# Kernel optimization log

Measured on AMD Instinct MI355X. Metric: run time of the kernel, lower is better.

Reference implementation:

```python
import jax, jax.numpy as jnp
import numpy as np

NUM_HEADS = 14
SCALE = 0.125  # fixed constant in the source, not 1/sqrt(head_dim)
PATCH = 14
DIM = 3 * PATCH * PATCH  # 588


def setup_inputs() -> dict:
    key = jax.random.key(0)
    k_x, k_cw, k_cb, k_qw, k_qb = jax.random.split(key, 5)
    B, C_in, H, W = 8, 3, 448, 448
    x = jax.random.normal(k_x, (B, C_in, H, W), dtype=jnp.float32)
    # Conv2d(in_channels=3, dim, kernel=patch, stride=patch), torch layout OIHW
    fan_in = C_in * PATCH * PATCH
    bound = 1.0 / np.sqrt(fan_in)
    conv_w = jax.random.uniform(k_cw, (DIM, C_in, PATCH, PATCH), jnp.float32, -bound, bound)
    conv_b = jax.random.uniform(k_cb, (DIM,), jnp.float32, -bound, bound)
    # Linear(dim, 3*dim): weight [out, in] torch layout
    lb = 1.0 / np.sqrt(DIM)
    qkv_w = jax.random.uniform(k_qw, (3 * DIM, DIM), jnp.float32, -lb, lb)
    qkv_b = jax.random.uniform(k_qb, (3 * DIM,), jnp.float32, -lb, lb)
    return {"x": x, "conv_w": conv_w, "conv_b": conv_b, "qkv_w": qkv_w, "qkv_b": qkv_b}


def reference(x, conv_w, conv_b, qkv_w, qkv_b):
    # Patch embedding: conv kernel==stride==patch  -> [B, DIM, H/p, W/p]
    y = jax.lax.conv_general_dilated(
        x, conv_w, window_strides=(PATCH, PATCH), padding="VALID",
        dimension_numbers=("NCHW", "OIHW", "NCHW"))
    y = y + conv_b[None, :, None, None]
    B = y.shape[0]
    # flatten(2).transpose(1, 2) -> [B, N, C]
    tokens = y.reshape(B, DIM, -1).transpose(0, 2, 1)
    N, C = tokens.shape[1], tokens.shape[2]
    hd = C // NUM_HEADS  # 42
    qkv = tokens @ qkv_w.T + qkv_b  # [B, N, 3C]
    qkv = qkv.reshape(B, N, 3, NUM_HEADS, hd).transpose(2, 0, 3, 1, 4)  # [3,B,H,N,hd]
    q, k, v = qkv[0], qkv[1], qkv[2]
    attn = jnp.einsum("bhnd,bhmd->bhnm", q, k) * SCALE  # [B,H,N,N]
    attn = jax.nn.softmax(attn, axis=-1)
    out = jnp.einsum("bhnm,bhmd->bhnd", attn, v)  # [B,H,N,hd]
    out = out.transpose(0, 2, 1, 3).reshape(B, N, C)  # [B,N,C]
    return out
```

## Files before the change

kernel.cpp:

```cpp
#include <hip/hip_runtime.h>

typedef unsigned short u16;
typedef unsigned int u32;
typedef __attribute__((ext_vector_type(8))) short bf16x8;
typedef __attribute__((ext_vector_type(4))) float f32x4;

#define MTOK 8192
#define KP   640
#define CC   588
#define C3   1764
#define NH   14
#define SEQ  1024
#define HD   42
#define DP   64
#define DV   48
#define SC2f 0.18033688011112042f

static __device__ __forceinline__ u16 f2b(float f) {
  unsigned u = __builtin_bit_cast(unsigned, f);
  u = (u + 0x7FFFu + ((u >> 16) & 1u)) >> 16;
  return (u16)u;
}

static __device__ __forceinline__ void gl_lds16(const void* g, void* l) {
  auto gp = (const unsigned int __attribute__((address_space(1)))*)((unsigned long long)g);
  auto lp = (unsigned int __attribute__((address_space(3)))*)((unsigned long long)l);
  __builtin_amdgcn_global_load_lds(gp, lp, 16, 0, 0);
}

static __device__ __forceinline__ u32 pk2(float lo, float hi) {
  u32 a = __builtin_bit_cast(u32, lo) + 0x8000u;
  u32 b = __builtin_bit_cast(u32, hi) + 0x8000u;
  return __builtin_amdgcn_perm(b, a, 0x07060302u);
}

__global__ void im2col_k(const float* __restrict__ x, u16* __restrict__ A) {
  int t = blockIdx.x;
  int b = t >> 10, pi = t & 1023, ph = pi >> 5, pw = pi & 31;
  const float* xb = x + (size_t)b * 3 * 448 * 448;
  for (int kk = threadIdx.x; kk < KP; kk += 256) {
    float v = 0.f;
    if (kk < CC) {
      int c = kk / 196, rem = kk - c * 196, i = rem / 14, j = rem - i * 14;
      v = xb[(size_t)(c * 448 + ph * 14 + i) * 448 + pw * 14 + j];
    }
    A[(size_t)t * KP + kk] = f2b(v);
  }
}

__global__ void padw_k(const float* __restrict__ w, u16* __restrict__ dst, int R) {
  int r = blockIdx.x;
  for (int c = threadIdx.x; c < KP; c += 256) {
    float v = (r < R && c < CC) ? w[(size_t)r * CC + c] : 0.f;
    dst[(size_t)r * KP + c] = f2b(v);
  }
}

template <int MODE>
__global__ void __launch_bounds__(256, 2) gemm_k(
    const u16* __restrict__ A, const u16* __restrict__ Bt,
    const float* __restrict__ bias, u16* __restrict__ out0,
    u16* __restrict__ qb, u16* __restrict__ kb, u16* __restrict__ vb) {
  __shared__ alignas(16) u16 sA[128 * 64];
  __shared__ alignas(16) u16 sB[128 * 64];
  const int tid = threadIdx.x;
  const int wave = tid >> 6, lane = tid & 63, quad = lane >> 4, l16 = lane & 15;
  const int wi = wave >> 1, wj = wave & 1;
  const int m0 = blockIdx.x * 128, n0 = blockIdx.y * 128;
  const int rL = lane >> 3, scid = lane & 7;
  const f32x4 z4 = {0.f, 0.f, 0.f, 0.f};

  f32x4 acc[4][4];
#pragma unroll
  for (int i = 0; i < 4; i++)
#pragma unroll
    for (int j = 0; j < 4; j++) acc[i][j] = z4;

  for (int k0 = 0; k0 < KP; k0 += 64) {
    __syncthreads();
#pragma unroll
    for (int cc = wave; cc < 16; cc += 4) {
      int r = cc * 8 + rL;
      gl_lds16(A + ((size_t)(m0 + r) * KP + k0 + (scid ^ (r & 7)) * 8), &sA[cc * 512]);
    }
#pragma unroll
    for (int cc = wave; cc < 16; cc += 4) {
      int r = cc * 8 + rL;
      gl_lds16(Bt + ((size_t)(n0 + r) * KP + k0 + (scid ^ (r & 7)) * 8), &sB[cc * 512]);
    }
    __syncthreads();
#pragma unroll
    for (int ks = 0; ks < 2; ks++) {
      bf16x8 af[4], bfr[4];
#pragma unroll
      for (int i = 0; i < 4; i++) {
        int r = wi * 64 + i * 16 + l16;
        af[i] = *(const bf16x8*)&sA[r * 64 + (((ks * 4 + quad) ^ (r & 7)) * 8)];
      }
#pragma unroll
      for (int j = 0; j < 4; j++) {
        int r = wj * 64 + j * 16 + l16;
        bfr[j] = *(const bf16x8*)&sB[r * 64 + (((ks * 4 + quad) ^ (r & 7)) * 8)];
      }
#pragma unroll
      for (int i = 0; i < 4; i++)
#pragma unroll
        for (int j = 0; j < 4; j++)
          acc[i][j] = __builtin_amdgcn_mfma_f32_16x16x32_bf16(af[i], bfr[j], acc[i][j], 0, 0, 0);
    }
  }

  const int baser = wi * 64 + quad * 4;
  if (MODE == 0) {
#pragma unroll
    for (int j = 0; j < 4; j++) {
      int col = n0 + wj * 64 + j * 16 + l16;
      float bs = (col < CC) ? bias[col] : 0.f;
#pragma unroll
      for (int i = 0; i < 4; i++) {
        int row = m0 + baser + i * 16;
#pragma unroll
        for (int r = 0; r < 4; r++)
          out0[(size_t)(row + r) * KP + col] = f2b(acc[i][j][r] + bs);
      }
    }
  } else {
#pragma unroll
    for (int j = 0; j < 4; j++) {
      int col = n0 + wj * 64 + j * 16 + l16;
      if (col < C3) {
        float bs = bias[col];
        int which = col / CC;
        int rem = col - which * CC;
        int h = rem / HD;
        int d = rem - h * HD;
        u16* dst = (which == 0) ? qb : (which == 1) ? kb : vb;
        float sc = (which == 0) ? SC2f : 1.0f;
#pragma unroll
        for (int i = 0; i < 4; i++) {
          int row = m0 + baser + i * 16;
#pragma unroll
          for (int r = 0; r < 4; r++) {
            int rw = row + r;
            int b = rw >> 10, n = rw & 1023;
            dst[((size_t)((b * NH + h) * SEQ + n)) * DP + d] = f2b((acc[i][j][r] + bs) * sc);
          }
        }
      }
    }
  }
}

__global__ void vtrans_k(const u16* __restrict__ vb, u16* __restrict__ vT) {
  __shared__ u16 tile[64 * 49];
  int bh = blockIdx.x, mt = blockIdx.y;
  for (int idx = threadIdx.x; idx < 64 * DV; idx += 256) {
    int n = idx / DV, d = idx - n * DV;
    u16 v = 0;
    if (d < HD) v = vb[((size_t)(bh * SEQ + mt * 64 + n)) * DP + d];
    tile[n * 49 + d] = v;
  }
  __syncthreads();
  for (int idx = threadIdx.x; idx < DV * 64; idx += 256) {
    int d = idx >> 6, n = idx & 63;
    u16 v = (d < HD) ? tile[n * 49 + d] : ((d == HD) ? (u16)0x3F80 : (u16)0);
    vT[((size_t)(bh * DV + d)) * SEQ + mt * 64 + n] = v;
  }
}

__global__ void __launch_bounds__(256) attn_k(
    const u16* __restrict__ qb, const u16* __restrict__ kb,
    const u16* __restrict__ vT, float* __restrict__ out) {
  __shared__ alignas(16) u16 sP[4][64 * 72];
  const int tid = threadIdx.x;
  const int wave = tid >> 6, lane = tid & 63, quad = lane >> 4, l16 = lane & 15;
  const int g = blockIdx.x;
  const int bh = (g & 7) * 14 + (g >> 5);
  const int qt = (g >> 3) & 3;
  const int q0 = qt * 256;
  const f32x4 z4 = {0.f, 0.f, 0.f, 0.f};
  u16* sPw = sP[wave];

  bf16x8 aq[4][2];
#pragma unroll
  for (int i = 0; i < 4; i++) {
    const u16* qrow = qb + ((size_t)(bh * SEQ + q0 + wave * 64 + i * 16 + l16)) * DP;
    aq[i][0] = *(const bf16x8*)&qrow[quad * 8];
    aq[i][1] = *(const bf16x8*)&qrow[32 + quad * 8];
  }
  f32x4 o[4][3];
#pragma unroll
  for (int i = 0; i < 4; i++)
#pragma unroll
    for (int j = 0; j < 3; j++) o[i][j] = z4;

  const u16* kb0 = kb + (size_t)bh * SEQ * DP;
  const u16* vb0 = vT + (size_t)bh * DV * SEQ;

  bf16x8 bk[4][2];
  bf16x8 bv[2][3];
#define LOADK(m0_)                                                                       \
  {                                                                                      \
    _Pragma("unroll") for (int j = 0; j < 4; j++) {                                      \
      const u16* kr = kb0 + ((size_t)((m0_) + 4 * l16 + j)) * DP + quad * 8;             \
      bk[j][0] = *(const bf16x8*)kr;                                                     \
      bk[j][1] = *(const bf16x8*)(kr + 32);                                              \
    }                                                                                    \
  }
#define LOADV(m0_)                                                                       \
  {                                                                                      \
    _Pragma("unroll") for (int ks = 0; ks < 2; ks++)                                     \
    _Pragma("unroll") for (int j = 0; j < 3; j++)                                        \
      bv[ks][j] = *(const bf16x8*)(vb0 + (size_t)(j * 16 + l16) * SEQ + (m0_) + ks * 32 + quad * 8); \
  }
  LOADK(0);
  LOADV(0);

  for (int kt = 0; kt < 16; kt++) {
    const int m1 = ((kt + 1) & 15) * 64;
#pragma unroll
    for (int i = 0; i < 4; i++) {
      f32x4 s[4];
#pragma unroll
      for (int j = 0; j < 4; j++) {
        f32x4 t = __builtin_amdgcn_mfma_f32_16x16x32_bf16(aq[i][0], bk[j][0], z4, 0, 0, 0);
        s[j] = __builtin_amdgcn_mfma_f32_16x16x32_bf16(aq[i][1], bk[j][1], t, 0, 0, 0);
      }
#pragma unroll
      for (int r = 0; r < 4; r++) {
        u32 d0 = pk2(__builtin_amdgcn_exp2f(s[0][r]), __builtin_amdgcn_exp2f(s[1][r]));
        u32 d1 = pk2(__builtin_amdgcn_exp2f(s[2][r]), __builtin_amdgcn_exp2f(s[3][r]));
        u32* dst = (u32*)&sPw[(i * 16 + quad * 4 + r) * 72 + l16 * 4];
        dst[0] = d0;
        dst[1] = d1;
      }
    }
    LOADK(m1);
#pragma unroll
    for (int ks = 0; ks < 2; ks++) {
#pragma unroll
      for (int i = 0; i < 4; i++) {
        bf16x8 ap = *(const bf16x8*)&sPw[(i * 16 + l16) * 72 + ks * 32 + quad * 8];
#pragma unroll
        for (int j = 0; j < 3; j++)
          o[i][j] = __builtin_amdgcn_mfma_f32_16x16x32_bf16(ap, bv[ks][j], o[i][j], 0, 0, 0);
      }
    }
    LOADV(m1);
  }

  const int b = bh / NH, h = bh - b * NH;
#pragma unroll
  for (int i = 0; i < 4; i++) {
#pragma unroll
    for (int r = 0; r < 4; r++) {
      float ls = __shfl(o[i][2][r], (lane & 48) + 10, 64);
      float rc = 1.f / ls;
      int row = wave * 64 + i * 16 + quad * 4 + r;
      float* orow = out + ((size_t)(b * SEQ + q0 + row)) * CC + h * HD;
#pragma unroll
      for (int j = 0; j < 3; j++) {
        int d = j * 16 + l16;
        if (d < HD) orow[d] = o[i][j][r] * rc;
      }
    }
  }
#undef LOADK
#undef LOADV
}

extern "C" void kernel_launch(void* const* d_in, const int* in_sizes, int n_in,
                              void* d_out, int out_size, void* d_ws, size_t ws_size,
                              hipStream_t stream) {
  (void)in_sizes; (void)n_in; (void)out_size; (void)ws_size;
  const float* x      = (const float*)d_in[0];
  const float* conv_w = (const float*)d_in[1];
  const float* conv_b = (const float*)d_in[2];
  const float* qkv_w  = (const float*)d_in[3];
  const float* qkv_b  = (const float*)d_in[4];
  float* out = (float*)d_out;

  char* ws = (char*)d_ws;
  size_t off = 0;
  u16* A      = (u16*)(ws + off); off += (size_t)MTOK * KP * 2;
  u16* Wc     = (u16*)(ws + off); off += (size_t)640 * KP * 2;
  u16* Wq     = (u16*)(ws + off); off += (size_t)1792 * KP * 2;
  u16* tokens = (u16*)(ws + off); off += (size_t)MTOK * KP * 2;
  u16* qbuf   = (u16*)(ws + off); off += (size_t)112 * SEQ * DP * 2;
  u16* kbuf   = (u16*)(ws + off); off += (size_t)112 * SEQ * DP * 2;
  u16* vbuf   = (u16*)(ws + off); off += (size_t)112 * SEQ * DP * 2;
  u16* vTb    = (u16*)(ws + off); off += (size_t)112 * DV * SEQ * 2;

  hipMemsetAsync(kbuf, 0, (size_t)112 * SEQ * DP * 2, stream);
  im2col_k<<<MTOK, 256, 0, stream>>>(x, A);
  padw_k<<<640, 256, 0, stream>>>(conv_w, Wc, CC);
  padw_k<<<1792, 256, 0, stream>>>(qkv_w, Wq, C3);
  gemm_k<0><<<dim3(64, 5), 256, 0, stream>>>(A, Wc, conv_b, tokens, nullptr, nullptr, nullptr);
  gemm_k<1><<<dim3(64, 14), 256, 0, stream>>>(tokens, Wq, qkv_b, nullptr, qbuf, kbuf, vbuf);
  vtrans_k<<<dim3(112, 16), 256, 0, stream>>>(vbuf, vTb);
  attn_k<<<448, 256, 0, stream>>>(qbuf, kbuf, vTb, out);
}
```

Baseline: 205.7 us.

## Stage K/V tiles in shared LDS and halve query rows per block

The attention kernel now loads each 64-key K tile and V tile once per block into swizzled LDS using direct global-to-LDS loads, and all four waves read from it. Before, each wave loaded K/V from global into registers on its own. Query rows per block drop from 256 to 128, which doubles the grid to 896 blocks for better occupancy and fewer registers. The cost is two __syncthreads per key tile, the loss of the register prefetch that overlapped the next tile's loads with compute, and K/V traffic repeated across twice as many blocks.

```diff
diff --git a/kernel.cpp b/kernel.cpp
--- a/kernel.cpp
+++ b/kernel.cpp
@@ -171,55 +171,62 @@
 __global__ void __launch_bounds__(256) attn_k(
     const u16* __restrict__ qb, const u16* __restrict__ kb,
     const u16* __restrict__ vT, float* __restrict__ out) {
-  __shared__ alignas(16) u16 sP[4][64 * 72];
+  __shared__ alignas(16) u16 sK[64 * 64];
+  __shared__ alignas(16) u16 sV[DV * 64];
+  __shared__ alignas(16) u16 sP[4][32 * 72];
   const int tid = threadIdx.x;
   const int wave = tid >> 6, lane = tid & 63, quad = lane >> 4, l16 = lane & 15;
   const int g = blockIdx.x;
-  const int bh = (g & 7) * 14 + (g >> 5);
-  const int qt = (g >> 3) & 3;
-  const int q0 = qt * 256;
+  const int bh = (g & 7) * 14 + (g >> 6);
+  const int qt = (g >> 3) & 7;
+  const int q0 = qt * 128;
+  const int rL = lane >> 3, scid = lane & 7;
   const f32x4 z4 = {0.f, 0.f, 0.f, 0.f};
   u16* sPw = sP[wave];
 
-  bf16x8 aq[4][2];
-#pragma unroll
-  for (int i = 0; i < 4; i++) {
-    const u16* qrow = qb + ((size_t)(bh * SEQ + q0 + wave * 64 + i * 16 + l16)) * DP;
+  bf16x8 aq[2][2];
+#pragma unroll
+  for (int i = 0; i < 2; i++) {
+    const u16* qrow = qb + ((size_t)(bh * SEQ + q0 + wave * 32 + i * 16 + l16)) * DP;
     aq[i][0] = *(const bf16x8*)&qrow[quad * 8];
     aq[i][1] = *(const bf16x8*)&qrow[32 + quad * 8];
   }
-  f32x4 o[4][3];
-#pragma unroll
-  for (int i = 0; i < 4; i++)
+  f32x4 o[2][3];
+#pragma unroll
+  for (int i = 0; i < 2; i++)
 #pragma unroll
     for (int j = 0; j < 3; j++) o[i][j] = z4;
 
   const u16* kb0 = kb + (size_t)bh * SEQ * DP;
   const u16* vb0 = vT + (size_t)bh * DV * SEQ;
 
-  bf16x8 bk[4][2];
-  bf16x8 bv[2][3];
-#define LOADK(m0_)                                                                       \
-  {                                                                                      \
-    _Pragma("unroll") for (int j = 0; j < 4; j++) {                                      \
-      const u16* kr = kb0 + ((size_t)((m0_) + 4 * l16 + j)) * DP + quad * 8;             \
-      bk[j][0] = *(const bf16x8*)kr;                                                     \
-      bk[j][1] = *(const bf16x8*)(kr + 32);                                              \
-    }                                                                                    \
-  }
-#define LOADV(m0_)                                                                       \
-  {                                                                                      \
-    _Pragma("unroll") for (int ks = 0; ks < 2; ks++)                                     \
-    _Pragma("unroll") for (int j = 0; j < 3; j++)                                        \
-      bv[ks][j] = *(const bf16x8*)(vb0 + (size_t)(j * 16 + l16) * SEQ + (m0_) + ks * 32 + quad * 8); \
-  }
-  LOADK(0);
-  LOADV(0);
-
   for (int kt = 0; kt < 16; kt++) {
-    const int m1 = ((kt + 1) & 15) * 64;
-#pragma unroll
-    for (int i = 0; i < 4; i++) {
+    const int m0 = kt * 64;
+    __syncthreads();
+    {
+      const u16* ktile = kb0 + (size_t)m0 * DP;
+#pragma unroll
+      for (int cc = wave; cc < 8; cc += 4) {
+        int r = cc * 8 + rL;
+        gl_lds16(ktile + ((size_t)r * 64 + (scid ^ ((r >> 2) & 7)) * 8), &sK[cc * 512]);
+      }
+#pragma unroll
+      for (int cc = wave; cc < 6; cc += 4) {
+        int d = cc * 8 + rL;
+        gl_lds16(vb0 + ((size_t)d * SEQ + m0 + (scid ^ (d & 7)) * 8), &sV[cc * 512]);
+      }
+    }
+    __syncthreads();
+    bf16x8 bk[4][2];
+#pragma unroll
+    for (int j = 0; j < 4; j++) {
+      int rr = 4 * l16 + j;
+#pragma unroll
+      for (int ks = 0; ks < 2; ks++)
+        bk[j][ks] = *(const bf16x8*)&sK[rr * 64 + (((ks * 4 + quad) ^ (l16 & 7)) * 8)];
+    }
+#pragma unroll
+    for (int i = 0; i < 2; i++) {
       f32x4 s[4];
 #pragma unroll
       for (int j = 0; j < 4; j++) {
@@ -235,28 +242,32 @@
         dst[1] = d1;
       }
     }
-    LOADK(m1);
 #pragma unroll
     for (int ks = 0; ks < 2; ks++) {
-#pragma unroll
-      for (int i = 0; i < 4; i++) {
+      bf16x8 bv[3];
+#pragma unroll
+      for (int j = 0; j < 3; j++) {
+        int d = j * 16 + l16;
+        bv[j] = *(const bf16x8*)&sV[d * 64 + (((ks * 4 + quad) ^ (d & 7)) * 8)];
+      }
+#pragma unroll
+      for (int i = 0; i < 2; i++) {
         bf16x8 ap = *(const bf16x8*)&sPw[(i * 16 + l16) * 72 + ks * 32 + quad * 8];
 #pragma unroll
         for (int j = 0; j < 3; j++)
-          o[i][j] = __builtin_amdgcn_mfma_f32_16x16x32_bf16(ap, bv[ks][j], o[i][j], 0, 0, 0);
-      }
-    }
-    LOADV(m1);
+          o[i][j] = __builtin_amdgcn_mfma_f32_16x16x32_bf16(ap, bv[j], o[i][j], 0, 0, 0);
+      }
+    }
   }
 
   const int b = bh / NH, h = bh - b * NH;
 #pragma unroll
-  for (int i = 0; i < 4; i++) {
+  for (int i = 0; i < 2; i++) {
 #pragma unroll
     for (int r = 0; r < 4; r++) {
       float ls = __shfl(o[i][2][r], (lane & 48) + 10, 64);
       float rc = 1.f / ls;
-      int row = wave * 64 + i * 16 + quad * 4 + r;
+      int row = wave * 32 + i * 16 + quad * 4 + r;
       float* orow = out + ((size_t)(b * SEQ + q0 + row)) * CC + h * HD;
 #pragma unroll
       for (int j = 0; j < 3; j++) {
@@ -265,8 +276,6 @@
       }
     }
   }
-#undef LOADK
-#undef LOADV
 }
 
 extern "C" void kernel_launch(void* const* d_in, const int* in_sizes, int n_in,
@@ -298,5 +307,5 @@
   gemm_k<0><<<dim3(64, 5), 256, 0, stream>>>(A, Wc, conv_b, tokens, nullptr, nullptr, nullptr);
   gemm_k<1><<<dim3(64, 14), 256, 0, stream>>>(tokens, Wq, qkv_b, nullptr, qbuf, kbuf, vbuf);
   vtrans_k<<<dim3(112, 16), 256, 0, stream>>>(vbuf, vTb);
-  attn_k<<<448, 256, 0, stream>>>(qbuf, kbuf, vTb, out);
-}
+  attn_k<<<896, 256, 0, stream>>>(qbuf, kbuf, vTb, out);
+}
```

Result: faster. 193.7 us (-5.8%).
